# Kernel tuning notes

Measured on AMD Instinct MI355X. Metric: run time of the kernel, lower is better.

## Reference

```python
import jax, jax.numpy as jnp
import numpy as np

MAX_WAVELENGTH = 1000.0

def _sine_pos(n, d):
    # keras_nlp SinePositionEncoding with max_wavelength=1000
    pos = jnp.arange(n, dtype=jnp.float32)
    i = jnp.arange(d)
    timescales = (1.0 / MAX_WAVELENGTH) ** ((2 * (i // 2)).astype(jnp.float32) / d)
    ang = pos[:, None] * timescales[None, :]  # (n, d)
    return jnp.where(i % 2 == 0, jnp.sin(ang), jnp.cos(ang))


def setup_inputs() -> dict:
    key = jax.random.key(0)
    ks = jax.random.split(key, 6)
    B, N, D, H, O = 4, 2048, 512, 8, 64
    inputs = jax.random.normal(ks[0], (B, N, D), jnp.float32)
    mem = jax.random.normal(ks[1], (B, H, O, O), jnp.float32) * 0.02
    # z accumulates sums of (elu(k)+1) > 0, so keep it positive
    z = jax.random.uniform(ks[2], (B, H, O), jnp.float32) + 1.0
    attn_kernel = jax.random.normal(ks[3], (D, H, O, 3), jnp.float32) * (1.0 / np.sqrt(D))
    out_kernel = jax.random.normal(ks[4], (O, H, O), jnp.float32) * (1.0 / np.sqrt(O * H))
    beta = jnp.zeros((1,), jnp.float32)
    return dict(inputs=inputs, mem=mem, z=z, attn_kernel=attn_kernel,
                out_kernel=out_kernel, beta=beta)


def reference(inputs, mem, z, attn_kernel, out_kernel, beta):
    B, N, D = inputs.shape
    x = inputs + _sine_pos(N, D)[None].astype(inputs.dtype)
    # fused QKV projection: (B,N,H,dims,3)
    kvq = jnp.einsum('bni,ihok->bnhok', x, attn_kernel)
    k, v, q = kvq[..., 0], kvq[..., 1], kvq[..., 2]
    # linear-attention memory readout
    q_elu = jax.nn.elu(q) + 1.0
    num = jnp.einsum('bhdo,bnhd->bnho', mem, q_elu)
    den = jnp.einsum('bhd,bnhd->bnh', z, q_elu)[..., None] + 1e-8
    A_mem = num / den
    # delta-rule state update
    k_elu = jax.nn.elu(k) + 1.0
    next_mem = mem + jnp.einsum('bnhz,bnho->bhzo', k_elu, v - A_mem)
    next_z = z + k_elu.sum(axis=1)
    # causal softmax attention over the chunk
    scale = jnp.sqrt(jnp.asarray(D, inputs.dtype))
    qk = jnp.einsum('bnho,bkho->bhnk', q, k) / scale
    mask = -(1.0 - jnp.tril(jnp.ones((N, N), inputs.dtype))) * 1e10
    A_soft = jax.nn.softmax(qk + mask, axis=-1)
    A_dot = jnp.einsum('bhnk,bkho->bnho', A_soft, v)
    # sigmoid-gated mix + output projection
    g = jax.nn.sigmoid(beta)  # (1,) broadcasts
    A = g * A_mem + (1.0 - g) * A_dot
    out = jnp.einsum('bnhi,iho->bno', A, out_kernel)
    return out, next_mem, next_z
```

## Files before the change

### kernel.cpp

```cpp
#include <hip/hip_runtime.h>
#include <hip/hip_bf16.h>
#include <math.h>

#define BB 4
#define SEQ 2048
#define DIM 512
#define NH 8
#define HD 64

typedef __attribute__((ext_vector_type(8))) short short8;
typedef __attribute__((ext_vector_type(4))) float f32x4;

static __device__ inline ushort f2bf(float f) {
    __hip_bfloat16 h = __float2bfloat16(f);
    union { __hip_bfloat16 h; ushort u; } cv;
    cv.h = h;
    return cv.u;
}
static __device__ inline float bf2f(ushort u) {
    return __uint_as_float((uint)u << 16);
}

#define GLOAD16(g, l)                                                          \
    __builtin_amdgcn_global_load_lds(                                          \
        (const __attribute__((address_space(1))) uint32_t*)(g),                \
        (__attribute__((address_space(3))) uint32_t*)(l), 16, 0, 0)

__global__ __launch_bounds__(256) void pos_add_bf16_kernel(const float* __restrict__ in,
                                                           ushort* __restrict__ xbf) {
    int idx = blockIdx.x * 256 + threadIdx.x;
    int p = idx & 255;
    int n = (idx >> 8) & 2047;
    float e = (float)(2 * p) * (1.0f / 512.0f);
    float ts = __expf(-6.907755278982137f * e);
    float arev = (float)n * (ts * 0.15915494309189535f);
    float f = arev - floorf(arev);
    float s = __builtin_amdgcn_sinf(f);
    float c = __builtin_amdgcn_cosf(f);
    float2 v = *(const float2*)(in + (size_t)idx * 2);
    uint pack = (uint)f2bf(v.x + s) | ((uint)f2bf(v.y + c) << 16);
    ((uint*)xbf)[idx] = pack;
}

__global__ __launch_bounds__(256) void wconv_kernel(const float* __restrict__ w,
                                                    ushort* __restrict__ wt) {
    __shared__ float tile[64][129];
    int ib = blockIdx.x;
    int jb = blockIdx.y;
    int t = threadIdx.x;
    #pragma unroll
    for (int u = 0; u < 8; ++u) {
        int idx = u * 1024 + t * 4;
        int r = idx >> 7, j = idx & 127;
        float4 v = *(const float4*)(w + (size_t)(ib * 64 + r) * 1536 + jb * 128 + j);
        tile[r][j] = v.x; tile[r][j + 1] = v.y; tile[r][j + 2] = v.z; tile[r][j + 3] = v.w;
    }
    __syncthreads();
    int j = t >> 1;
    int rh = (t & 1) * 32;
    int jg = jb * 128 + j;
    int h = jg / 192;
    int rem = jg - h * 192;
    int o = rem / 3;
    int c = rem - o * 3;
    int nrow = c * 512 + h * 64 + o;
    #pragma unroll
    for (int s8 = 0; s8 < 4; ++s8) {
        short8 pk;
        #pragma unroll
        for (int q = 0; q < 8; ++q) pk[q] = (short)f2bf(tile[rh + s8 * 8 + q][j]);
        *(short8*)(wt + (size_t)nrow * 512 + ib * 64 + rh + s8 * 8) = pk;
    }
}

__global__ __launch_bounds__(256) void wout_conv_kernel(const float* __restrict__ wo,
                                                        ushort* __restrict__ wobf) {
    int g = blockIdx.x * 256 + threadIdx.x;
    int o2 = g >> 9, k = g & 511;
    int h = k >> 6, i = k & 63;
    wobf[g] = f2bf(wo[(size_t)i * 512 + h * 64 + o2]);
}

__global__ __launch_bounds__(256) void qkv_mfma_kernel(const ushort* __restrict__ xbf,
                                                       const ushort* __restrict__ wt,
                                                       ushort* __restrict__ kbf,
                                                       ushort* __restrict__ vbf,
                                                       ushort* __restrict__ qbf) {
    __shared__ __align__(16) ushort As[128 * 64];
    __shared__ __align__(16) ushort Bs[128 * 64];
    int t = threadIdx.x;
    int w = t >> 6, lane = t & 63, l15 = lane & 15, lg = lane >> 4;
    int wr = w >> 1, wc = w & 1;
    int m0 = blockIdx.x * 128;
    int by = blockIdx.y;
    int n0 = by * 128;
    int sw = l15 & 7;
    f32x4 acc[4][4] = {};

    int rowp[4], colp[4];
    #pragma unroll
    for (int p = 0; p < 4; ++p) {
        int ch = t + 256 * p;
        rowp[p] = ch >> 3;
        colp[p] = (((ch & 7) ^ (rowp[p] & 7))) * 8;
    }

    for (int k0 = 0; k0 < 512; k0 += 64) {
        __syncthreads();
        #pragma unroll
        for (int p = 0; p < 4; ++p)
            GLOAD16(xbf + (size_t)(m0 + rowp[p]) * 512 + k0 + colp[p], As + (t + 256 * p) * 8);
        #pragma unroll
        for (int p = 0; p < 4; ++p)
            GLOAD16(wt + (size_t)(n0 + rowp[p]) * 512 + k0 + colp[p], Bs + (t + 256 * p) * 8);
        __syncthreads();
        #pragma unroll
        for (int ks = 0; ks < 2; ++ks) {
            short8 af[4], bf[4];
            #pragma unroll
            for (int mi = 0; mi < 4; ++mi)
                af[mi] = *(const short8*)&As[(wr * 64 + mi * 16 + l15) * 64 + ((ks * 4 + lg) ^ sw) * 8];
            #pragma unroll
            for (int ni = 0; ni < 4; ++ni)
                bf[ni] = *(const short8*)&Bs[(wc * 64 + ni * 16 + l15) * 64 + ((ks * 4 + lg) ^ sw) * 8];
            #pragma unroll
            for (int mi = 0; mi < 4; ++mi)
                #pragma unroll
                for (int ni = 0; ni < 4; ++ni)
                    acc[mi][ni] = __builtin_amdgcn_mfma_f32_16x16x32_bf16(af[mi], bf[ni], acc[mi][ni], 0, 0, 0);
        }
    }

    ushort* dst = (by < 4) ? kbf : (by < 8) ? vbf : qbf;
    int ho0 = (by & 3) * 128 + wc * 64;
    int mb = m0 + wr * 64;
    #pragma unroll
    for (int mi = 0; mi < 4; ++mi)
        #pragma unroll
        for (int ni = 0; ni < 4; ++ni)
            #pragma unroll
            for (int r = 0; r < 4; ++r)
                dst[(size_t)(mb + mi * 16 + lg * 4 + r) * 512 + ho0 + ni * 16 + l15] =
                    f2bf(acc[mi][ni][r]);
}

__global__ __launch_bounds__(256) void vt_kernel(const ushort* __restrict__ vbf,
                                                 ushort* __restrict__ vtbf) {
    int bid = blockIdx.x;
    int nt = bid & 31;
    int bh = bid >> 5;
    int b = bh >> 3, h = bh & 7;
    __shared__ ushort tile[64][72];
    int t = threadIdx.x;
    {
        int n = t >> 2, dc = (t & 3) * 16;
        const ushort* src = vbf + (size_t)(b * 2048 + nt * 64 + n) * 512 + h * 64 + dc;
        *(short8*)&tile[n][dc] = *(const short8*)src;
        *(short8*)&tile[n][dc + 8] = *(const short8*)(src + 8);
    }
    __syncthreads();
    {
        int d = t >> 2, nc = (t & 3) * 16;
        ushort* dst = vtbf + (size_t)bh * 64 * 2048 + (size_t)d * 2048 + nt * 64 + nc;
        short8 a, bq;
        #pragma unroll
        for (int j = 0; j < 8; ++j) { a[j] = (short)tile[nc + j][d]; bq[j] = (short)tile[nc + 8 + j][d]; }
        *(short8*)dst = a;
        *(short8*)(dst + 8) = bq;
    }
}

__global__ __launch_bounds__(256) void amem_mfma_kernel(const ushort* __restrict__ qbf,
                                                        const float* __restrict__ mem,
                                                        const float* __restrict__ zin,
                                                        ushort* __restrict__ ambf) {
    int bid = blockIdx.x;
    int nt = bid & 7;
    int h = (bid >> 3) & 7;
    int b = bid >> 6;
    __shared__ __align__(16) ushort bt_s[80 * 64];
    int t = threadIdx.x;
    int w = t >> 6, lane = t & 63, l15 = lane & 15, lg = lane >> 4;

    {
        int d = t >> 2;
        int o0 = (t & 3) * 16;
        const float* msrc = mem + (size_t)(b * 8 + h) * 4096 + (size_t)d * 64 + o0;
        #pragma unroll
        for (int j = 0; j < 16; ++j) {
            int o = o0 + j;
            int c = (d >> 3) ^ (o & 7);
            bt_s[(o * 8 + c) * 8 + (d & 7)] = f2bf(msrc[j]);
        }
        if (t < 64) {
            bt_s[(64 * 8 + (t >> 3)) * 8 + (t & 7)] = f2bf(zin[(b * 8 + h) * 64 + t]);
        }
    }
    __syncthreads();

    int sw = l15 & 7;
    short8 bfr[5][2];
    #pragma unroll
    for (int n = 0; n < 5; ++n) {
        const ushort* br = &bt_s[(n * 16 + l15) * 64];
        bfr[n][0] = *(const short8*)&br[(lg ^ sw) * 8];
        bfr[n][1] = *(const short8*)&br[((4 + lg) ^ sw) * 8];
    }

    int rowbase = b * 2048 + nt * 256 + w * 64;
    f32x4 acc[4][5] = {};
    #pragma unroll
    for (int m = 0; m < 4; ++m) {
        const ushort* qrow = qbf + (size_t)(rowbase + m * 16 + l15) * 512 + h * 64;
        short8 q0 = *(const short8*)(qrow + lg * 8);
        short8 q1 = *(const short8*)(qrow + 32 + lg * 8);
        short8 a0, a1;
        #pragma unroll
        for (int j = 0; j < 8; ++j) {
            float f0 = bf2f((ushort)q0[j]);
            float f1 = bf2f((ushort)q1[j]);
            a0[j] = (short)f2bf(f0 > 0.f ? f0 + 1.f : __expf(f0));
            a1[j] = (short)f2bf(f1 > 0.f ? f1 + 1.f : __expf(f1));
        }
        #pragma unroll
        for (int n = 0; n < 5; ++n) {
            acc[m][n] = __builtin_amdgcn_mfma_f32_16x16x32_bf16(a0, bfr[n][0], acc[m][n], 0, 0, 0);
            acc[m][n] = __builtin_amdgcn_mfma_f32_16x16x32_bf16(a1, bfr[n][1], acc[m][n], 0, 0, 0);
        }
    }

    #pragma unroll
    for (int m = 0; m < 4; ++m) {
        float inv[4];
        #pragma unroll
        for (int r = 0; r < 4; ++r) {
            float d = __shfl(acc[m][4][r], (lane & 48));
            inv[r] = 1.f / (d + 1e-8f);
        }
        #pragma unroll
        for (int r = 0; r < 4; ++r) {
            ushort* dst = ambf + (size_t)(rowbase + m * 16 + lg * 4 + r) * 512 + h * 64;
            #pragma unroll
            for (int n = 0; n < 4; ++n)
                dst[n * 16 + l15] = f2bf(acc[m][n][r] * inv[r]);
        }
    }
}

__global__ __launch_bounds__(256) void delta_part_kernel(const ushort* __restrict__ kbf,
                                                         const ushort* __restrict__ vbf,
                                                         const ushort* __restrict__ ambf,
                                                         float* __restrict__ part,
                                                         float* __restrict__ zpart) {
    int bid = blockIdx.x;
    int bh = bid & 31;
    int chunk = bid >> 5;
    int h = bh & 7, b = bh >> 3;
    __shared__ __align__(16) float ke_s[2048];
    __shared__ __align__(16) float vm_s[2048];
    int t = threadIdx.x;
    int tx = t & 15, ty = t >> 4;
    float acc[4][4] = {};
    float nz = 0.f;
    int nbase = chunk * 256;
    for (int n0 = 0; n0 < 256; n0 += 32) {
        {
            int nn = t >> 3, cc = (t & 7) * 8;
            size_t g = (size_t)(b * 2048 + nbase + n0 + nn) * 512 + h * 64 + cc;
            short8 k8 = *(const short8*)(kbf + g);
            short8 v8 = *(const short8*)(vbf + g);
            short8 a8 = *(const short8*)(ambf + g);
            #pragma unroll
            for (int j = 0; j < 8; ++j) {
                float kv = bf2f((ushort)k8[j]);
                ke_s[t * 8 + j] = kv > 0.f ? kv + 1.f : __expf(kv);
                vm_s[t * 8 + j] = bf2f((ushort)v8[j]) - bf2f((ushort)a8[j]);
            }
        }
        __syncthreads();
        #pragma unroll
        for (int nn = 0; nn < 32; ++nn) {
            float4 ka4 = *(const float4*)&ke_s[nn * 64 + ty * 4];
            float4 vv4 = *(const float4*)&vm_s[nn * 64 + tx * 4];
            float ka[4] = {ka4.x, ka4.y, ka4.z, ka4.w};
            float vv[4] = {vv4.x, vv4.y, vv4.z, vv4.w};
            #pragma unroll
            for (int i = 0; i < 4; ++i)
                #pragma unroll
                for (int j = 0; j < 4; ++j) acc[i][j] += ka[i] * vv[j];
        }
        if (t < 64) {
            #pragma unroll
            for (int nn = 0; nn < 32; ++nn) nz += ke_s[nn * 64 + t];
        }
        __syncthreads();
    }
    float* pdst = part + (size_t)bid * 4096;
    #pragma unroll
    for (int i = 0; i < 4; ++i)
        #pragma unroll
        for (int j = 0; j < 4; ++j)
            pdst[(ty * 4 + i) * 64 + tx * 4 + j] = acc[i][j];
    if (t < 64) zpart[bid * 64 + t] = nz;
}

__global__ __launch_bounds__(256) void delta_reduce_kernel(const float* __restrict__ part,
                                                           const float* __restrict__ zpart,
                                                           const float* __restrict__ mem,
                                                           const float* __restrict__ zin,
                                                           float* __restrict__ out_mem,
                                                           float* __restrict__ out_z) {
    int bh = blockIdx.x;
    int t = threadIdx.x;
    #pragma unroll
    for (int q = 0; q < 4; ++q) {
        int e = t * 16 + q * 4;
        float4 acc = *(const float4*)(mem + (size_t)bh * 4096 + e);
        #pragma unroll
        for (int c = 0; c < 8; ++c) {
            float4 pv = *(const float4*)(part + (size_t)(c * 32 + bh) * 4096 + e);
            acc.x += pv.x; acc.y += pv.y; acc.z += pv.z; acc.w += pv.w;
        }
        *(float4*)(out_mem + (size_t)bh * 4096 + e) = acc;
    }
    if (t < 64) {
        float z = zin[bh * 64 + t];
        #pragma unroll
        for (int c = 0; c < 8; ++c) z += zpart[(c * 32 + bh) * 64 + t];
        out_z[bh * 64 + t] = z;
    }
}

#define FL_PSTR 72
__global__ __launch_bounds__(256, 2) void flash4_kernel(const ushort* __restrict__ qbf,
                                                        const ushort* __restrict__ kbf,
                                                        const ushort* __restrict__ vtbf,
                                                        ushort* __restrict__ adbf) {
    int bid0 = blockIdx.x;
    int bid = (bid0 & 7) * 64 + (bid0 >> 3);
    int i = bid & 15;
    int h = (bid >> 4) & 7;
    int b = bid >> 7;
    __shared__ __align__(16) ushort k_s[2][4096];
    __shared__ __align__(16) ushort vt_s[2][4096];
    __shared__ __align__(16) ushort p_s[4][16 * FL_PSTR];
    int t = threadIdx.x;
    int w = t >> 6, lane = t & 63, l15 = lane & 15, lg = lane >> 4;
    const int rA = i, rB = 31 - i;
    const int sw = l15 & 7;
    const float C = 0.06375875f;

    const ushort* qbase = qbf + (size_t)(b * 2048) * 512 + h * 64 + lg * 8;
    short8 qfA[2], qfB[2];
    #pragma unroll
    for (int c = 0; c < 2; ++c) {
        short8 ra = *(const short8*)(qbase + (size_t)(rA * 64 + w * 16 + l15) * 512 + c * 32);
        short8 rb = *(const short8*)(qbase + (size_t)(rB * 64 + w * 16 + l15) * 512 + c * 32);
        #pragma unroll
        for (int j = 0; j < 8; ++j) {
            qfA[c][j] = (short)f2bf(bf2f((ushort)ra[j]) * C);
            qfB[c][j] = (short)f2bf(bf2f((ushort)rb[j]) * C);
        }
    }
    f32x4 oA[4] = {}, oB[4] = {};
    f32x4 lA = {0.f, 0.f, 0.f, 0.f}, lB = {0.f, 0.f, 0.f, 0.f};

    int ch0 = t, ch1 = t + 256;
    int row0 = ch0 >> 3, sc0 = (ch0 & 7) ^ (row0 & 7);
    int row1 = ch1 >> 3, sc1 = (ch1 & 7) ^ (row1 & 7);
    const ushort* kbase = kbf + (size_t)(b * 2048) * 512 + h * 64;
    const ushort* vtbase = vtbf + (size_t)(b * 8 + h) * 64 * 2048;
    ushort* pw = &p_s[w][0];

    short8 ones;
    #pragma unroll
    for (int j = 0; j < 8; ++j) ones[j] = (short)0x3F80;

    short8 kf[4][2], vf[4][2];

    auto STAGE = [&](int buf, int kt) {
        GLOAD16(kbase + (size_t)(kt * 64 + row0) * 512 + sc0 * 8, &k_s[buf][ch0 * 8]);
        GLOAD16(kbase + (size_t)(kt * 64 + row1) * 512 + sc1 * 8, &k_s[buf][ch1 * 8]);
        GLOAD16(vtbase + (size_t)row0 * 2048 + kt * 64 + sc0 * 8, &vt_s[buf][ch0 * 8]);
        GLOAD16(vtbase + (size_t)row1 * 2048 + kt * 64 + sc1 * 8, &vt_s[buf][ch1 * 8]);
    };

    auto proc = [&](const short8* qf, f32x4* oo, f32x4& ll, int rt, int kt) {
        f32x4 s[4];
        #pragma unroll
        for (int t4 = 0; t4 < 4; ++t4) {
            f32x4 z = {0.f, 0.f, 0.f, 0.f};
            z = __builtin_amdgcn_mfma_f32_16x16x32_bf16(qf[0], kf[t4][0], z, 0, 0, 0);
            z = __builtin_amdgcn_mfma_f32_16x16x32_bf16(qf[1], kf[t4][1], z, 0, 0, 0);
            s[t4] = z;
        }
        if (kt == rt) {
            #pragma unroll
            for (int t4 = 0; t4 < 4; ++t4) {
                int colb = t4 * 16 + l15;
                int rowb = w * 16 + lg * 4;
                #pragma unroll
                for (int r = 0; r < 4; ++r)
                    if (colb > rowb + r) s[t4][r] = -1e30f;
            }
        }
        #pragma unroll
        for (int t4 = 0; t4 < 4; ++t4)
            #pragma unroll
            for (int r = 0; r < 4; ++r)
                pw[(lg * 4 + r) * FL_PSTR + t4 * 16 + l15] =
                    f2bf(__builtin_amdgcn_exp2f(s[t4][r]));
        short8 pf0 = *(const short8*)&pw[l15 * FL_PSTR + lg * 8];
        short8 pf1 = *(const short8*)&pw[l15 * FL_PSTR + 32 + lg * 8];
        ll = __builtin_amdgcn_mfma_f32_16x16x32_bf16(pf0, ones, ll, 0, 0, 0);
        ll = __builtin_amdgcn_mfma_f32_16x16x32_bf16(pf1, ones, ll, 0, 0, 0);
        #pragma unroll
        for (int dt = 0; dt < 4; ++dt) {
            oo[dt] = __builtin_amdgcn_mfma_f32_16x16x32_bf16(pf0, vf[dt][0], oo[dt], 0, 0, 0);
            oo[dt] = __builtin_amdgcn_mfma_f32_16x16x32_bf16(pf1, vf[dt][1], oo[dt], 0, 0, 0);
        }
    };

    STAGE(0, 0);
    for (int kt = 0; kt <= rB; ++kt) {
        int cur = kt & 1;
        __builtin_amdgcn_s_barrier();
        if (kt < rB) {
            STAGE(cur ^ 1, kt + 1);
            asm volatile("s_waitcnt vmcnt(4)" ::: "memory");
        } else {
            asm volatile("s_waitcnt vmcnt(0)" ::: "memory");
        }
        __builtin_amdgcn_s_barrier();
        #pragma unroll
        for (int t4 = 0; t4 < 4; ++t4) {
            const ushort* kr = &k_s[cur][(t4 * 16 + l15) * 64];
            kf[t4][0] = *(const short8*)&kr[(lg ^ sw) * 8];
            kf[t4][1] = *(const short8*)&kr[((4 + lg) ^ sw) * 8];
            const ushort* vr = &vt_s[cur][(t4 * 16 + l15) * 64];
            vf[t4][0] = *(const short8*)&vr[(lg ^ sw) * 8];
            vf[t4][1] = *(const short8*)&vr[((4 + lg) ^ sw) * 8];
        }
        proc(qfB, oB, lB, rB, kt);
        if (kt <= rA) proc(qfA, oA, lA, rA, kt);
    }

    auto fin = [&](f32x4* oo, f32x4& ll, int rt) {
        #pragma unroll
        for (int r = 0; r < 4; ++r) {
            float inv = 1.f / ll[r];
            ushort* dst = adbf + (size_t)(b * 2048 + rt * 64 + w * 16 + lg * 4 + r) * 512 + h * 64;
            #pragma unroll
            for (int dt = 0; dt < 4; ++dt)
                dst[dt * 16 + l15] = f2bf(oo[dt][r] * inv);
        }
    };
    fin(oA, lA, rA);
    fin(oB, lB, rB);
}

__global__ __launch_bounds__(256) void outproj_mfma_kernel(const ushort* __restrict__ ambf,
                                                           const ushort* __restrict__ adbf,
                                                           const ushort* __restrict__ wobf,
                                                           const float* __restrict__ beta,
                                                           float* __restrict__ out) {
    __shared__ __align__(16) ushort W_s[64 * 512];
    __shared__ __align__(16) ushort A_s[32 * 64];
    int t = threadIdx.x;
    int w = t >> 6, lane = t & 63, l15 = lane & 15, lg = lane >> 4;
    int msub = w & 1, nh = w >> 1;
    int m0 = blockIdx.x * 32;
    float g = 1.f / (1.f + __expf(-beta[0]));
    float gi = 1.f - g;

    #pragma unroll
    for (int p = 0; p < 16; ++p) {
        int ch = p * 256 + t;
        int row = ch >> 6, c = ch & 63;
        int cs = c ^ (row & 7);
        GLOAD16(wobf + (size_t)row * 512 + cs * 8, W_s + ch * 8);
    }

    int ar = t >> 3, ac = t & 7;
    int sw = l15 & 7;
    f32x4 acc[2] = {};

    for (int ks = 0; ks < 8; ++ks) {
        size_t gofs = (size_t)(m0 + ar) * 512 + ks * 64 + ac * 8;
        short8 a8 = *(const short8*)(ambf + gofs);
        short8 d8 = *(const short8*)(adbf + gofs);
        short8 x0;
        #pragma unroll
        for (int j = 0; j < 8; ++j)
            x0[j] = (short)f2bf(g * bf2f((ushort)a8[j]) + gi * bf2f((ushort)d8[j]));
        if (ks) __syncthreads();
        *(short8*)&A_s[(ar * 8 + (ac ^ (ar & 7))) * 8] = x0;
        __syncthreads();

        const ushort* arow = &A_s[(msub * 16 + l15) * 64];
        short8 af0 = *(const short8*)&arow[(lg ^ sw) * 8];
        short8 af1 = *(const short8*)&arow[((4 + lg) ^ sw) * 8];
        #pragma unroll
        for (int ni = 0; ni < 2; ++ni) {
            const ushort* wrow = &W_s[(nh * 32 + ni * 16 + l15) * 512];
            short8 bf0 = *(const short8*)&wrow[(ks * 8 + (lg ^ sw)) * 8];
            short8 bf1 = *(const short8*)&wrow[(ks * 8 + ((4 + lg) ^ sw)) * 8];
            acc[ni] = __builtin_amdgcn_mfma_f32_16x16x32_bf16(af0, bf0, acc[ni], 0, 0, 0);
            acc[ni] = __builtin_amdgcn_mfma_f32_16x16x32_bf16(af1, bf1, acc[ni], 0, 0, 0);
        }
    }

    #pragma unroll
    for (int ni = 0; ni < 2; ++ni)
        #pragma unroll
        for (int r = 0; r < 4; ++r)
            out[(size_t)(m0 + msub * 16 + lg * 4 + r) * 64 + nh * 32 + ni * 16 + l15] = acc[ni][r];
}

extern "C" void kernel_launch(void* const* d_in, const int* in_sizes, int n_in,
                              void* d_out, int out_size, void* d_ws, size_t ws_size,
                              hipStream_t stream) {
    const float* inputs = (const float*)d_in[0];
    const float* mem    = (const float*)d_in[1];
    const float* zin    = (const float*)d_in[2];
    const float* attnk  = (const float*)d_in[3];
    const float* outk   = (const float*)d_in[4];
    const float* beta   = (const float*)d_in[5];
    float* out = (float*)d_out;
    float* ws  = (float*)d_ws;

    ushort* am_bf = (ushort*)ws;
    ushort* ad_bf = (ushort*)(ws + 2097152);
    ushort* kbf   = (ushort*)(ws + 4194304);
    ushort* vbf   = (ushort*)(ws + 6291456);
    ushort* qbf   = (ushort*)(ws + 8388608);
    ushort* vtbf  = (ushort*)(ws + 10485760);
    ushort* xbf   = (ushort*)(ws + 12582912);
    ushort* wtbf  = (ushort*)(ws + 14680064);
    ushort* wobf  = (ushort*)(ws + 15073280);
    float*  part  = ws + 15089664;
    float*  zpart = ws + 16138240;

    float* out_main = out;
    float* out_mem  = out + 524288;
    float* out_z    = out + 655360;

    pos_add_bf16_kernel<<<8192, 256, 0, stream>>>(inputs, xbf);
    wconv_kernel<<<dim3(8, 12), 256, 0, stream>>>(attnk, wtbf);
    wout_conv_kernel<<<128, 256, 0, stream>>>(outk, wobf);
    qkv_mfma_kernel<<<dim3(64, 12), 256, 0, stream>>>(xbf, wtbf, kbf, vbf, qbf);
    vt_kernel<<<1024, 256, 0, stream>>>(vbf, vtbf);
    amem_mfma_kernel<<<256, 256, 0, stream>>>(qbf, mem, zin, am_bf);
    delta_part_kernel<<<256, 256, 0, stream>>>(kbf, vbf, am_bf, part, zpart);
    delta_reduce_kernel<<<32, 256, 0, stream>>>(part, zpart, mem, zin, out_mem, out_z);
    flash4_kernel<<<512, 256, 0, stream>>>(qbf, kbf, vtbf, ad_bf);
    outproj_mfma_kernel<<<256, 256, 0, stream>>>(am_bf, ad_bf, wobf, beta, out_main);
}
```

Measured before the change: 183.9 us.

## Use LDS transpose reads for V and P in flash attention, drop V transpose kernel

New measurement: 180.3 us. 1.02x faster.

```diff
diff --git a/kernel.cpp b/kernel.cpp
--- a/kernel.cpp
+++ b/kernel.cpp
@@ -10,6 +10,8 @@
 
 typedef __attribute__((ext_vector_type(8))) short short8;
 typedef __attribute__((ext_vector_type(4))) float f32x4;
+typedef __attribute__((ext_vector_type(2))) unsigned int u32x2;
+typedef __attribute__((address_space(3))) const ushort lds_cushort;
 
 static __device__ inline ushort f2bf(float f) {
     __hip_bfloat16 h = __float2bfloat16(f);
@@ -25,6 +27,12 @@
     __builtin_amdgcn_global_load_lds(                                          \
         (const __attribute__((address_space(1))) uint32_t*)(g),                \
         (__attribute__((address_space(3))) uint32_t*)(l), 16, 0, 0)
+
+static __device__ __forceinline__ u32x2 tr16_b64(lds_cushort* p) {
+    u32x2 r;
+    asm volatile("ds_read_b64_tr_b16 %0, %1" : "=v"(r) : "v"(p) : "memory");
+    return r;
+}
 
 __global__ __launch_bounds__(256) void pos_add_bf16_kernel(const float* __restrict__ in,
                                                            ushort* __restrict__ xbf) {
@@ -42,43 +50,45 @@
     ((uint*)xbf)[idx] = pack;
 }
 
-__global__ __launch_bounds__(256) void wconv_kernel(const float* __restrict__ w,
-                                                    ushort* __restrict__ wt) {
-    __shared__ float tile[64][129];
-    int ib = blockIdx.x;
-    int jb = blockIdx.y;
-    int t = threadIdx.x;
-    #pragma unroll
-    for (int u = 0; u < 8; ++u) {
-        int idx = u * 1024 + t * 4;
-        int r = idx >> 7, j = idx & 127;
-        float4 v = *(const float4*)(w + (size_t)(ib * 64 + r) * 1536 + jb * 128 + j);
-        tile[r][j] = v.x; tile[r][j + 1] = v.y; tile[r][j + 2] = v.z; tile[r][j + 3] = v.w;
-    }
-    __syncthreads();
-    int j = t >> 1;
-    int rh = (t & 1) * 32;
-    int jg = jb * 128 + j;
-    int h = jg / 192;
-    int rem = jg - h * 192;
-    int o = rem / 3;
-    int c = rem - o * 3;
-    int nrow = c * 512 + h * 64 + o;
-    #pragma unroll
-    for (int s8 = 0; s8 < 4; ++s8) {
-        short8 pk;
-        #pragma unroll
-        for (int q = 0; q < 8; ++q) pk[q] = (short)f2bf(tile[rh + s8 * 8 + q][j]);
-        *(short8*)(wt + (size_t)nrow * 512 + ib * 64 + rh + s8 * 8) = pk;
-    }
-}
-
-__global__ __launch_bounds__(256) void wout_conv_kernel(const float* __restrict__ wo,
-                                                        ushort* __restrict__ wobf) {
-    int g = blockIdx.x * 256 + threadIdx.x;
-    int o2 = g >> 9, k = g & 511;
-    int h = k >> 6, i = k & 63;
-    wobf[g] = f2bf(wo[(size_t)i * 512 + h * 64 + o2]);
+__global__ __launch_bounds__(256) void wprep_kernel(const float* __restrict__ w,
+                                                    ushort* __restrict__ wt,
+                                                    const float* __restrict__ wo,
+                                                    ushort* __restrict__ wobf) {
+    int bid = blockIdx.x;
+    int t = threadIdx.x;
+    if (bid < 96) {
+        __shared__ float tile[64][129];
+        int ib = bid & 7;
+        int jb = bid >> 3;
+        #pragma unroll
+        for (int u = 0; u < 8; ++u) {
+            int idx = u * 1024 + t * 4;
+            int r = idx >> 7, j = idx & 127;
+            float4 v = *(const float4*)(w + (size_t)(ib * 64 + r) * 1536 + jb * 128 + j);
+            tile[r][j] = v.x; tile[r][j + 1] = v.y; tile[r][j + 2] = v.z; tile[r][j + 3] = v.w;
+        }
+        __syncthreads();
+        int j = t >> 1;
+        int rh = (t & 1) * 32;
+        int jg = jb * 128 + j;
+        int h = jg / 192;
+        int rem = jg - h * 192;
+        int o = rem / 3;
+        int c = rem - o * 3;
+        int nrow = c * 512 + h * 64 + o;
+        #pragma unroll
+        for (int s8 = 0; s8 < 4; ++s8) {
+            short8 pk;
+            #pragma unroll
+            for (int q = 0; q < 8; ++q) pk[q] = (short)f2bf(tile[rh + s8 * 8 + q][j]);
+            *(short8*)(wt + (size_t)nrow * 512 + ib * 64 + rh + s8 * 8) = pk;
+        }
+    } else {
+        int g = (bid - 96) * 256 + t;
+        int o2 = g >> 9, k = g & 511;
+        int h = k >> 6, i = k & 63;
+        wobf[g] = f2bf(wo[(size_t)i * 512 + h * 64 + o2]);
+    }
 }
 
 __global__ __launch_bounds__(256) void qkv_mfma_kernel(const ushort* __restrict__ xbf,
@@ -142,32 +152,6 @@
             for (int r = 0; r < 4; ++r)
                 dst[(size_t)(mb + mi * 16 + lg * 4 + r) * 512 + ho0 + ni * 16 + l15] =
                     f2bf(acc[mi][ni][r]);
-}
-
-__global__ __launch_bounds__(256) void vt_kernel(const ushort* __restrict__ vbf,
-                                                 ushort* __restrict__ vtbf) {
-    int bid = blockIdx.x;
-    int nt = bid & 31;
-    int bh = bid >> 5;
-    int b = bh >> 3, h = bh & 7;
-    __shared__ ushort tile[64][72];
-    int t = threadIdx.x;
-    {
-        int n = t >> 2, dc = (t & 3) * 16;
-        const ushort* src = vbf + (size_t)(b * 2048 + nt * 64 + n) * 512 + h * 64 + dc;
-        *(short8*)&tile[n][dc] = *(const short8*)src;
-        *(short8*)&tile[n][dc + 8] = *(const short8*)(src + 8);
-    }
-    __syncthreads();
-    {
-        int d = t >> 2, nc = (t & 3) * 16;
-        ushort* dst = vtbf + (size_t)bh * 64 * 2048 + (size_t)d * 2048 + nt * 64 + nc;
-        short8 a, bq;
-        #pragma unroll
-        for (int j = 0; j < 8; ++j) { a[j] = (short)tile[nc + j][d]; bq[j] = (short)tile[nc + 8 + j][d]; }
-        *(short8*)dst = a;
-        *(short8*)(dst + 8) = bq;
-    }
 }
 
 __global__ __launch_bounds__(256) void amem_mfma_kernel(const ushort* __restrict__ qbf,
@@ -331,10 +315,9 @@
     }
 }
 
-#define FL_PSTR 72
-__global__ __launch_bounds__(256, 2) void flash4_kernel(const ushort* __restrict__ qbf,
+__global__ __launch_bounds__(256, 2) void flash5_kernel(const ushort* __restrict__ qbf,
                                                         const ushort* __restrict__ kbf,
-                                                        const ushort* __restrict__ vtbf,
+                                                        const ushort* __restrict__ vbf,
                                                         ushort* __restrict__ adbf) {
     int bid0 = blockIdx.x;
     int bid = (bid0 & 7) * 64 + (bid0 >> 3);
@@ -342,8 +325,8 @@
     int h = (bid >> 4) & 7;
     int b = bid >> 7;
     __shared__ __align__(16) ushort k_s[2][4096];
-    __shared__ __align__(16) ushort vt_s[2][4096];
-    __shared__ __align__(16) ushort p_s[4][16 * FL_PSTR];
+    __shared__ __align__(16) ushort v_s[2][4096];
+    __shared__ __align__(16) ushort p_s[4][1024];
     int t = threadIdx.x;
     int w = t >> 6, lane = t & 63, l15 = lane & 15, lg = lane >> 4;
     const int rA = i, rB = 31 - i;
@@ -366,10 +349,12 @@
     f32x4 lA = {0.f, 0.f, 0.f, 0.f}, lB = {0.f, 0.f, 0.f, 0.f};
 
     int ch0 = t, ch1 = t + 256;
-    int row0 = ch0 >> 3, sc0 = (ch0 & 7) ^ (row0 & 7);
-    int row1 = ch1 >> 3, sc1 = (ch1 & 7) ^ (row1 & 7);
+    int krow0 = ch0 >> 3, ksc0 = (ch0 & 7) ^ (krow0 & 7);
+    int krow1 = ch1 >> 3, ksc1 = (ch1 & 7) ^ (krow1 & 7);
+    int vd0 = ch0 >> 7, vn0 = (ch0 >> 1) & 63, vh0 = ch0 & 1;
+    int vd1 = ch1 >> 7, vn1 = (ch1 >> 1) & 63, vh1 = ch1 & 1;
     const ushort* kbase = kbf + (size_t)(b * 2048) * 512 + h * 64;
-    const ushort* vtbase = vtbf + (size_t)(b * 8 + h) * 64 * 2048;
+    const ushort* vbase = vbf + (size_t)(b * 2048) * 512 + h * 64;
     ushort* pw = &p_s[w][0];
 
     short8 ones;
@@ -379,10 +364,10 @@
     short8 kf[4][2], vf[4][2];
 
     auto STAGE = [&](int buf, int kt) {
-        GLOAD16(kbase + (size_t)(kt * 64 + row0) * 512 + sc0 * 8, &k_s[buf][ch0 * 8]);
-        GLOAD16(kbase + (size_t)(kt * 64 + row1) * 512 + sc1 * 8, &k_s[buf][ch1 * 8]);
-        GLOAD16(vtbase + (size_t)row0 * 2048 + kt * 64 + sc0 * 8, &vt_s[buf][ch0 * 8]);
-        GLOAD16(vtbase + (size_t)row1 * 2048 + kt * 64 + sc1 * 8, &vt_s[buf][ch1 * 8]);
+        GLOAD16(kbase + (size_t)(kt * 64 + krow0) * 512 + ksc0 * 8, &k_s[buf][ch0 * 8]);
+        GLOAD16(kbase + (size_t)(kt * 64 + krow1) * 512 + ksc1 * 8, &k_s[buf][ch1 * 8]);
+        GLOAD16(vbase + (size_t)(kt * 64 + vn0) * 512 + vd0 * 16 + vh0 * 8, &v_s[buf][ch0 * 8]);
+        GLOAD16(vbase + (size_t)(kt * 64 + vn1) * 512 + vd1 * 16 + vh1 * 8, &v_s[buf][ch1 * 8]);
     };
 
     auto proc = [&](const short8* qf, f32x4* oo, f32x4& ll, int rt, int kt) {
@@ -405,13 +390,27 @@
             }
         }
         #pragma unroll
-        for (int t4 = 0; t4 < 4; ++t4)
+        for (int t4 = 0; t4 < 4; ++t4) {
+            union { ushort u[4]; u32x2 d; } pk;
             #pragma unroll
             for (int r = 0; r < 4; ++r)
-                pw[(lg * 4 + r) * FL_PSTR + t4 * 16 + l15] =
-                    f2bf(__builtin_amdgcn_exp2f(s[t4][r]));
-        short8 pf0 = *(const short8*)&pw[l15 * FL_PSTR + lg * 8];
-        short8 pf1 = *(const short8*)&pw[l15 * FL_PSTR + 32 + lg * 8];
+                pk.u[r] = f2bf(__builtin_amdgcn_exp2f(s[t4][r]));
+            *(u32x2*)&pw[(t4 * 16 + l15) * 16 + lg * 4] = pk.d;
+        }
+        u32x2 praw0, praw1, praw2, praw3;
+        {
+            lds_cushort* pb = (lds_cushort*)&pw[l15];
+            praw0 = tr16_b64(pb + (lg * 8 + 0) * 16);
+            praw1 = tr16_b64(pb + (lg * 8 + 4) * 16);
+            praw2 = tr16_b64(pb + (32 + lg * 8 + 0) * 16);
+            praw3 = tr16_b64(pb + (32 + lg * 8 + 4) * 16);
+        }
+        asm volatile("s_waitcnt lgkmcnt(0)" ::: "memory");
+        __builtin_amdgcn_sched_barrier(0);
+        union { u32x2 d[2]; short8 s8; } up0, up1;
+        up0.d[0] = praw0; up0.d[1] = praw1;
+        up1.d[0] = praw2; up1.d[1] = praw3;
+        short8 pf0 = up0.s8, pf1 = up1.s8;
         ll = __builtin_amdgcn_mfma_f32_16x16x32_bf16(pf0, ones, ll, 0, 0, 0);
         ll = __builtin_amdgcn_mfma_f32_16x16x32_bf16(pf1, ones, ll, 0, 0, 0);
         #pragma unroll
@@ -437,9 +436,25 @@
             const ushort* kr = &k_s[cur][(t4 * 16 + l15) * 64];
             kf[t4][0] = *(const short8*)&kr[(lg ^ sw) * 8];
             kf[t4][1] = *(const short8*)&kr[((4 + lg) ^ sw) * 8];
-            const ushort* vr = &vt_s[cur][(t4 * 16 + l15) * 64];
-            vf[t4][0] = *(const short8*)&vr[(lg ^ sw) * 8];
-            vf[t4][1] = *(const short8*)&vr[((4 + lg) ^ sw) * 8];
+        }
+        u32x2 vraw[4][4];
+        #pragma unroll
+        for (int dt = 0; dt < 4; ++dt) {
+            lds_cushort* vb = (lds_cushort*)&v_s[cur][dt * 1024 + l15];
+            vraw[dt][0] = tr16_b64(vb + (lg * 8 + 0) * 16);
+            vraw[dt][1] = tr16_b64(vb + (lg * 8 + 4) * 16);
+            vraw[dt][2] = tr16_b64(vb + (32 + lg * 8 + 0) * 16);
+            vraw[dt][3] = tr16_b64(vb + (32 + lg * 8 + 4) * 16);
+        }
+        asm volatile("s_waitcnt lgkmcnt(0)" ::: "memory");
+        __builtin_amdgcn_sched_barrier(0);
+        #pragma unroll
+        for (int dt = 0; dt < 4; ++dt) {
+            union { u32x2 d[2]; short8 s8; } u0, u1;
+            u0.d[0] = vraw[dt][0]; u0.d[1] = vraw[dt][1];
+            u1.d[0] = vraw[dt][2]; u1.d[1] = vraw[dt][3];
+            vf[dt][0] = u0.s8;
+            vf[dt][1] = u1.s8;
         }
         proc(qfB, oB, lB, rB, kt);
         if (kt <= rA) proc(qfA, oA, lA, rA, kt);
@@ -534,7 +549,6 @@
     ushort* kbf   = (ushort*)(ws + 4194304);
     ushort* vbf   = (ushort*)(ws + 6291456);
     ushort* qbf   = (ushort*)(ws + 8388608);
-    ushort* vtbf  = (ushort*)(ws + 10485760);
     ushort* xbf   = (ushort*)(ws + 12582912);
     ushort* wtbf  = (ushort*)(ws + 14680064);
     ushort* wobf  = (ushort*)(ws + 15073280);
@@ -546,13 +560,11 @@
     float* out_z    = out + 655360;
 
     pos_add_bf16_kernel<<<8192, 256, 0, stream>>>(inputs, xbf);
-    wconv_kernel<<<dim3(8, 12), 256, 0, stream>>>(attnk, wtbf);
-    wout_conv_kernel<<<128, 256, 0, stream>>>(outk, wobf);
+    wprep_kernel<<<224, 256, 0, stream>>>(attnk, wtbf, outk, wobf);
     qkv_mfma_kernel<<<dim3(64, 12), 256, 0, stream>>>(xbf, wtbf, kbf, vbf, qbf);
-    vt_kernel<<<1024, 256, 0, stream>>>(vbf, vtbf);
     amem_mfma_kernel<<<256, 256, 0, stream>>>(qbf, mem, zin, am_bf);
     delta_part_kernel<<<256, 256, 0, stream>>>(kbf, vbf, am_bf, part, zpart);
     delta_reduce_kernel<<<32, 256, 0, stream>>>(part, zpart, mem, zin, out_mem, out_z);
-    flash4_kernel<<<512, 256, 0, stream>>>(qbf, kbf, vtbf, ad_bf);
+    flash5_kernel<<<512, 256, 0, stream>>>(qbf, kbf, vbf, ad_bf);
     outproj_mfma_kernel<<<256, 256, 0, stream>>>(am_bf, ad_bf, wobf, beta, out_main);
 }
```
